# Performance work log

Hardware: AMD Instinct MI355X
Metric: run time of the kernel (lower is better)

## Reference

```python
import jax, jax.numpy as jnp
import numpy as np

TEMPERATURE = 8.0  # sqrt(d_head=64)
CLAMP = 15.0
EPS = 1e-6


def setup_inputs() -> dict:
    key = jax.random.key(0)
    kq, kk, kv, km = jax.random.split(key, 4)
    B, Lq, Lk, D = 16, 2048, 2048, 64
    q = jax.random.normal(kq, (B, Lq, D), dtype=jnp.float32)
    k = jax.random.normal(kk, (B, Lk, D), dtype=jnp.float32)
    v = jax.random.normal(kv, (B, Lk, D), dtype=jnp.float32)
    mask = jax.random.randint(km, (B, Lq, Lk), 0, 2).astype(jnp.float32)
    return {"q": q, "k": k, "v": v, "mask": mask}


def masked_softmax(x, m, axis=-1):
    # clamp -> multiply by mask -> stable exp -> multiply by mask -> normalize
    x = jnp.clip(x, -CLAMP, CLAMP)
    x = x * m
    e_x = jnp.exp(x - jnp.max(x, axis=axis, keepdims=True))
    e_x = e_x * m
    return e_x / (jnp.sum(e_x, axis=axis, keepdims=True) + EPS)


def reference(q, k, v, mask):
    # scores: [B, Lq, Lk]
    attn = jnp.einsum('bqd,bkd->bqk', q, k) / TEMPERATURE
    attn = masked_softmax(attn, mask, axis=2)
    # dropout is identity in eval mode (deterministic reference)
    output = jnp.einsum('bqk,bkd->bqd', attn, v)
    return (output, attn)
```

## Files before the change

### kernel.cpp

```cpp
#include <hip/hip_runtime.h>
#include <stdint.h>

#define NB 16
#define LQ 2048
#define LK 2048
#define DH 64
#define QT 16
#define NW 16
#define STRIP (NW * 16)
#define NIT (LK / STRIP)

typedef short bf16x8 __attribute__((ext_vector_type(8)));
typedef float f32x4 __attribute__((ext_vector_type(4)));

__device__ __forceinline__ unsigned short f2bf(float f) {
    union { float f; uint32_t u; } v; v.f = f;
    uint32_t u = v.u;
    u += 0x7FFFu + ((u >> 16) & 1u);
    return (unsigned short)(u >> 16);
}
__device__ __forceinline__ float bf2f(unsigned short h) {
    union { uint32_t u; float f; } v; v.u = ((uint32_t)h) << 16;
    return v.f;
}
__device__ __forceinline__ uint32_t pack2(float lo, float hi) {
    return (uint32_t)f2bf(lo) | ((uint32_t)f2bf(hi) << 16);
}

__global__ void convert_kernel(const float* __restrict__ q, const float* __restrict__ k,
                               const float* __restrict__ v,
                               unsigned short* __restrict__ qb,
                               unsigned short* __restrict__ kb,
                               unsigned short* __restrict__ vtb) {
    int bid = blockIdx.x;
    int tid = threadIdx.x;
    if (bid < 2048) {
        const float* src = (bid < 1024) ? q : k;
        unsigned short* dst = (bid < 1024) ? qb : kb;
        int64_t off = (int64_t)(bid & 1023) * 2048 + (int64_t)tid * 8;
        float4 a = *(const float4*)(src + off);
        float4 b4 = *(const float4*)(src + off + 4);
        uint4 o;
        o.x = pack2(a.x, a.y);
        o.y = pack2(a.z, a.w);
        o.z = pack2(b4.x, b4.y);
        o.w = pack2(b4.z, b4.w);
        *(uint4*)(dst + off) = o;
    } else {
        __shared__ unsigned short tile[64][72];
        int bid2 = bid - 2048;
        int bb = bid2 >> 5, kt = bid2 & 31;
        int k0 = kt * 64;
        int krow = tid >> 2, dc = (tid & 3) * 16;
        const float* vp = v + ((int64_t)(bb * LK) + k0 + krow) * DH + dc;
        float4 x0 = *(const float4*)(vp);
        float4 x1 = *(const float4*)(vp + 4);
        float4 x2 = *(const float4*)(vp + 8);
        float4 x3 = *(const float4*)(vp + 12);
        float vals[16] = {x0.x, x0.y, x0.z, x0.w, x1.x, x1.y, x1.z, x1.w,
                          x2.x, x2.y, x2.z, x2.w, x3.x, x3.y, x3.z, x3.w};
        #pragma unroll
        for (int i = 0; i < 16; ++i) tile[dc + i][krow] = f2bf(vals[i]);
        __syncthreads();
        int d = tid >> 2, kc = (tid & 3) * 16;
        uint4 r0 = *(const uint4*)&tile[d][kc];
        uint4 r1 = *(const uint4*)&tile[d][kc + 8];
        unsigned short* op = vtb + ((int64_t)(bb * DH) + d) * LK + k0 + kc;
        *(uint4*)op = r0;
        *(uint4*)(op + 8) = r1;
    }
}

__device__ __forceinline__ void ld_f32x4(f32x4& d, const float* p) {
    asm volatile("global_load_dwordx4 %0, %1, off" : "=v"(d) : "v"((uint64_t)p));
}
__device__ __forceinline__ void ld_bf16x8(bf16x8& d, const unsigned short* p) {
    asm volatile("global_load_dwordx4 %0, %1, off" : "=v"(d) : "v"((uint64_t)p));
}

__launch_bounds__(1024, 8)
__global__ void attn_kernel(const unsigned short* __restrict__ qb,
                            const unsigned short* __restrict__ kb,
                            const unsigned short* __restrict__ vtb,
                            const float* __restrict__ mask,
                            float* __restrict__ out, float* __restrict__ attn) {
    extern __shared__ char smem[];
    float* denom_part = (float*)(smem + QT * LK * 2);
    float* denF       = (float*)(smem + QT * LK * 2 + 1024);
    float* pp         = (float*)(smem + QT * LK * 2 + 1088);

    int bid = blockIdx.x;
    int swz = (bid & 7) * 256 + (bid >> 3);
    int b = swz >> 7;
    int q0 = (swz & 127) * QT;

    int tid = threadIdx.x;
    int lane = tid & 63;
    int wave = tid >> 6;
    int lr = lane & 15, lg = lane >> 4;

    bf16x8 qf0, qf1;
    {
        const unsigned short* qp = qb + ((int64_t)(b * LQ + q0 + lr)) * DH + 8 * lg;
        qf0 = *(const bf16x8*)qp;
        qf1 = *(const bf16x8*)(qp + 32);
    }

    float dsum = 0.f;

    {
        const unsigned short* kpw =
            kb + (int64_t)b * LK * DH + (wave * 16 + lr) * DH + 8 * lg;
        const float* mrow =
            mask + ((int64_t)(b * LQ + q0 + lr)) * LK + wave * 16 + lg * 4;

        f32x4  mk[3];
        bf16x8 ka[3], kb_[3];
        #pragma unroll
        for (int t = 0; t < 3; ++t) {
            ld_f32x4(mk[t], mrow + t * STRIP);
            ld_bf16x8(ka[t],  kpw + (int64_t)t * STRIP * DH);
            ld_bf16x8(kb_[t], kpw + (int64_t)t * STRIP * DH + 32);
        }
        #pragma unroll
        for (int kt = 0; kt < NIT; ++kt) {
            int s = kt % 3;
            if (kt < 6)
                asm volatile("s_waitcnt vmcnt(6)"
                             : "+v"(mk[s]), "+v"(ka[s]), "+v"(kb_[s]));
            else if (kt == 6)
                asm volatile("s_waitcnt vmcnt(3)"
                             : "+v"(mk[s]), "+v"(ka[s]), "+v"(kb_[s]));
            else
                asm volatile("s_waitcnt vmcnt(0)"
                             : "+v"(mk[s]), "+v"(ka[s]), "+v"(kb_[s]));
            __builtin_amdgcn_sched_barrier(0);

            f32x4 acc = {0.f, 0.f, 0.f, 0.f};
            acc = __builtin_amdgcn_mfma_f32_16x16x32_bf16(ka[s],  qf0, acc, 0, 0, 0);
            acc = __builtin_amdgcn_mfma_f32_16x16x32_bf16(kb_[s], qf1, acc, 0, 0, 0);
            unsigned short eb[4];
            #pragma unroll
            for (int j = 0; j < 4; ++j) {
                float sc = acc[j] * 0.125f;
                sc = fminf(fmaxf(sc, -15.0f), 15.0f);
                unsigned short p = f2bf(__expf(sc));
                eb[j] = (mk[s][j] != 0.f) ? p : (unsigned short)0;
                dsum += bf2f(eb[j]);
            }
            uint2 u;
            u.x = (uint32_t)eb[0] | ((uint32_t)eb[1] << 16);
            u.y = (uint32_t)eb[2] | ((uint32_t)eb[3] << 16);
            int c = kt * STRIP + wave * 16 + lg * 4;
            int byteoff = (lr * 4096 + c * 2) ^ ((lr & 7) << 4);
            *(uint2*)(smem + byteoff) = u;

            if (kt < NIT - 3) {
                ld_f32x4(mk[s], mrow + (kt + 3) * STRIP);
                ld_bf16x8(ka[s],  kpw + (int64_t)(kt + 3) * STRIP * DH);
                ld_bf16x8(kb_[s], kpw + (int64_t)(kt + 3) * STRIP * DH + 32);
            }
        }
    }

    dsum += __shfl_xor(dsum, 16);
    dsum += __shfl_xor(dsum, 32);
    if (lane < 16) denom_part[wave * 16 + lane] = dsum;
    __syncthreads();

    {
        int r = wave;
        float den = 1e-6f;
        #pragma unroll
        for (int w = 0; w < NW; ++w) den += denom_part[w * 16 + r];
        if (lane == 0) denF[r] = den;
        float inv = 1.0f / den;
        float* ap = attn + ((int64_t)(b * LQ + q0 + r)) * LK;
        int rowbase = r * 4096;
        int sw = (r & 7) << 4;
        int c0l = lane * 8;
        #pragma unroll
        for (int i = 0; i < 4; ++i) {
            int byteoff = (rowbase + (i * 512 + c0l) * 2) ^ sw;
            bf16x8 ev = *(const bf16x8*)(smem + byteoff);
            f32x4 o0, o1;
            o0[0] = bf2f((unsigned short)ev[0]) * inv;
            o0[1] = bf2f((unsigned short)ev[1]) * inv;
            o0[2] = bf2f((unsigned short)ev[2]) * inv;
            o0[3] = bf2f((unsigned short)ev[3]) * inv;
            o1[0] = bf2f((unsigned short)ev[4]) * inv;
            o1[1] = bf2f((unsigned short)ev[5]) * inv;
            o1[2] = bf2f((unsigned short)ev[6]) * inv;
            o1[3] = bf2f((unsigned short)ev[7]) * inv;
            *(f32x4*)(ap + i * 512 + c0l) = o0;
            *(f32x4*)(ap + i * 512 + c0l + 4) = o1;
        }
    }

    f32x4 pacc = {0.f, 0.f, 0.f, 0.f};
    int cw = (wave & 3) * 16, kq = wave >> 2;
    {
        const unsigned short* vp =
            vtb + ((int64_t)(b * DH + cw + lr)) * LK + kq * 512 + 8 * lg;
        int rowbase = lr * 4096;
        int sw = (lr & 7) << 4;
        int kk0 = kq * 512;
        #pragma unroll 4
        for (int kk = 0; kk < 512; kk += 32) {
            int byteoff = (rowbase + (kk0 + kk + 8 * lg) * 2) ^ sw;
            bf16x8 ef = *(const bf16x8*)(smem + byteoff);
            bf16x8 vf = *(const bf16x8*)(vp + kk);
            pacc = __builtin_amdgcn_mfma_f32_16x16x32_bf16(ef, vf, pacc, 0, 0, 0);
        }
    }
    if (kq != 0) {
        #pragma unroll
        for (int j = 0; j < 4; ++j)
            pp[((kq - 1) * 4 + (wave & 3)) * 256 + (lg * 4 + j) * 16 + lr] = pacc[j];
    }
    __syncthreads();
    if (kq == 0) {
        int c4 = wave & 3;
        #pragma unroll
        for (int j = 0; j < 4; ++j) {
            int r = lg * 4 + j;
            float den = denF[r];
            float val = pacc[j] + pp[(c4) * 256 + r * 16 + lr] +
                        pp[(4 + c4) * 256 + r * 16 + lr] +
                        pp[(8 + c4) * 256 + r * 16 + lr];
            out[((int64_t)(b * LQ + q0 + r)) * DH + cw + lr] = val / den;
        }
    }
}

extern "C" void kernel_launch(void* const* d_in, const int* in_sizes, int n_in,
                              void* d_out, int out_size, void* d_ws, size_t ws_size,
                              hipStream_t stream) {
    const float* q    = (const float*)d_in[0];
    const float* k    = (const float*)d_in[1];
    const float* v    = (const float*)d_in[2];
    const float* mask = (const float*)d_in[3];
    float* out  = (float*)d_out;
    float* attn = out + (int64_t)NB * LQ * DH;

    unsigned short* qb  = (unsigned short*)d_ws;
    unsigned short* kb  = qb + (int64_t)NB * LQ * DH;
    unsigned short* vtb = kb + (int64_t)NB * LK * DH;

    (void)hipFuncSetAttribute((const void*)attn_kernel,
                              hipFuncAttributeMaxDynamicSharedMemorySize, 78912);

    convert_kernel<<<2560, 256, 0, stream>>>(q, k, v, qb, kb, vtb);
    attn_kernel<<<2048, 1024, 78912, stream>>>(qb, kb, vtb, mask, out, attn);
}
```

Measured before the change: 215.6 us.

## Keep softmax probabilities in registers and shrink blocks to four waves

Blocks now run 4 waves instead of 16. Each wave owns a contiguous 512-key range and keeps its exponentiated scores packed in registers. The large shared-memory staging buffer is gone, and the P·V product uses 16x16x16 MFMA fed straight from the register scores, so the LDS round-trip and the extra barrier phase disappear. In exchange, register pressure rises (64 dwords of scores plus four accumulators per lane), V loads become narrower 8-byte reads, and each block has fewer waves to hide memory latency.

```diff
diff --git a/kernel.cpp b/kernel.cpp
--- a/kernel.cpp
+++ b/kernel.cpp
@@ -6,11 +6,10 @@
 #define LK 2048
 #define DH 64
 #define QT 16
-#define NW 16
-#define STRIP (NW * 16)
-#define NIT (LK / STRIP)
+#define NSTRIP 32
 
 typedef short bf16x8 __attribute__((ext_vector_type(8)));
+typedef short bf16x4 __attribute__((ext_vector_type(4)));
 typedef float f32x4 __attribute__((ext_vector_type(4)));
 
 __device__ __forceinline__ unsigned short f2bf(float f) {
@@ -78,16 +77,28 @@
     asm volatile("global_load_dwordx4 %0, %1, off" : "=v"(d) : "v"((uint64_t)p));
 }
 
-__launch_bounds__(1024, 8)
+__device__ __forceinline__ f32x4 pv_mfma(bf16x4 a, bf16x4 bfrag, f32x4 c) {
+#if defined(__has_builtin)
+#if __has_builtin(__builtin_amdgcn_mfma_f32_16x16x16bf16_1k)
+    return __builtin_amdgcn_mfma_f32_16x16x16bf16_1k(a, bfrag, c, 0, 0, 0);
+#else
+    asm("v_mfma_f32_16x16x16_bf16 %0, %1, %2, %0" : "+v"(c) : "v"(a), "v"(bfrag));
+    return c;
+#endif
+#else
+    asm("v_mfma_f32_16x16x16_bf16 %0, %1, %2, %0" : "+v"(c) : "v"(a), "v"(bfrag));
+    return c;
+#endif
+}
+
+__launch_bounds__(256, 4)
 __global__ void attn_kernel(const unsigned short* __restrict__ qb,
                             const unsigned short* __restrict__ kb,
                             const unsigned short* __restrict__ vtb,
                             const float* __restrict__ mask,
                             float* __restrict__ out, float* __restrict__ attn) {
-    extern __shared__ char smem[];
-    float* denom_part = (float*)(smem + QT * LK * 2);
-    float* denF       = (float*)(smem + QT * LK * 2 + 1024);
-    float* pp         = (float*)(smem + QT * LK * 2 + 1088);
+    __shared__ float den_part[4][16];
+    __shared__ float pp[3][4][16][16];
 
     int bid = blockIdx.x;
     int swz = (bid & 7) * 256 + (bid >> 3);
@@ -106,29 +117,30 @@
         qf1 = *(const bf16x8*)(qp + 32);
     }
 
+    const unsigned short* kpw =
+        kb + (int64_t)b * LK * DH + (wave * NSTRIP * 16 + lr) * DH + 8 * lg;
+    const float* mrow =
+        mask + ((int64_t)(b * LQ + q0 + lr)) * LK + wave * NSTRIP * 16 + lg * 4;
+
+    uint32_t es[2 * NSTRIP];
     float dsum = 0.f;
 
     {
-        const unsigned short* kpw =
-            kb + (int64_t)b * LK * DH + (wave * 16 + lr) * DH + 8 * lg;
-        const float* mrow =
-            mask + ((int64_t)(b * LQ + q0 + lr)) * LK + wave * 16 + lg * 4;
-
         f32x4  mk[3];
         bf16x8 ka[3], kb_[3];
         #pragma unroll
         for (int t = 0; t < 3; ++t) {
-            ld_f32x4(mk[t], mrow + t * STRIP);
-            ld_bf16x8(ka[t],  kpw + (int64_t)t * STRIP * DH);
-            ld_bf16x8(kb_[t], kpw + (int64_t)t * STRIP * DH + 32);
-        }
-        #pragma unroll
-        for (int kt = 0; kt < NIT; ++kt) {
+            ld_f32x4(mk[t], mrow + t * 16);
+            ld_bf16x8(ka[t],  kpw + (int64_t)t * 16 * DH);
+            ld_bf16x8(kb_[t], kpw + (int64_t)t * 16 * DH + 32);
+        }
+        #pragma unroll
+        for (int kt = 0; kt < NSTRIP; ++kt) {
             int s = kt % 3;
-            if (kt < 6)
+            if (kt < NSTRIP - 2)
                 asm volatile("s_waitcnt vmcnt(6)"
                              : "+v"(mk[s]), "+v"(ka[s]), "+v"(kb_[s]));
-            else if (kt == 6)
+            else if (kt == NSTRIP - 2)
                 asm volatile("s_waitcnt vmcnt(3)"
                              : "+v"(mk[s]), "+v"(ka[s]), "+v"(kb_[s]));
             else
@@ -148,87 +160,89 @@
                 eb[j] = (mk[s][j] != 0.f) ? p : (unsigned short)0;
                 dsum += bf2f(eb[j]);
             }
-            uint2 u;
-            u.x = (uint32_t)eb[0] | ((uint32_t)eb[1] << 16);
-            u.y = (uint32_t)eb[2] | ((uint32_t)eb[3] << 16);
-            int c = kt * STRIP + wave * 16 + lg * 4;
-            int byteoff = (lr * 4096 + c * 2) ^ ((lr & 7) << 4);
-            *(uint2*)(smem + byteoff) = u;
-
-            if (kt < NIT - 3) {
-                ld_f32x4(mk[s], mrow + (kt + 3) * STRIP);
-                ld_bf16x8(ka[s],  kpw + (int64_t)(kt + 3) * STRIP * DH);
-                ld_bf16x8(kb_[s], kpw + (int64_t)(kt + 3) * STRIP * DH + 32);
+            es[2 * kt]     = (uint32_t)eb[0] | ((uint32_t)eb[1] << 16);
+            es[2 * kt + 1] = (uint32_t)eb[2] | ((uint32_t)eb[3] << 16);
+
+            if (kt < NSTRIP - 3) {
+                ld_f32x4(mk[s], mrow + (kt + 3) * 16);
+                ld_bf16x8(ka[s],  kpw + (int64_t)(kt + 3) * 16 * DH);
+                ld_bf16x8(kb_[s], kpw + (int64_t)(kt + 3) * 16 * DH + 32);
             }
         }
     }
 
     dsum += __shfl_xor(dsum, 16);
     dsum += __shfl_xor(dsum, 32);
-    if (lane < 16) denom_part[wave * 16 + lane] = dsum;
+    if (lane < 16) den_part[wave][lane] = dsum;
     __syncthreads();
 
-    {
-        int r = wave;
-        float den = 1e-6f;
-        #pragma unroll
-        for (int w = 0; w < NW; ++w) den += denom_part[w * 16 + r];
-        if (lane == 0) denF[r] = den;
-        float inv = 1.0f / den;
-        float* ap = attn + ((int64_t)(b * LQ + q0 + r)) * LK;
-        int rowbase = r * 4096;
-        int sw = (r & 7) << 4;
-        int c0l = lane * 8;
-        #pragma unroll
-        for (int i = 0; i < 4; ++i) {
-            int byteoff = (rowbase + (i * 512 + c0l) * 2) ^ sw;
-            bf16x8 ev = *(const bf16x8*)(smem + byteoff);
-            f32x4 o0, o1;
-            o0[0] = bf2f((unsigned short)ev[0]) * inv;
-            o0[1] = bf2f((unsigned short)ev[1]) * inv;
-            o0[2] = bf2f((unsigned short)ev[2]) * inv;
-            o0[3] = bf2f((unsigned short)ev[3]) * inv;
-            o1[0] = bf2f((unsigned short)ev[4]) * inv;
-            o1[1] = bf2f((unsigned short)ev[5]) * inv;
-            o1[2] = bf2f((unsigned short)ev[6]) * inv;
-            o1[3] = bf2f((unsigned short)ev[7]) * inv;
-            *(f32x4*)(ap + i * 512 + c0l) = o0;
-            *(f32x4*)(ap + i * 512 + c0l + 4) = o1;
-        }
-    }
-
-    f32x4 pacc = {0.f, 0.f, 0.f, 0.f};
-    int cw = (wave & 3) * 16, kq = wave >> 2;
-    {
-        const unsigned short* vp =
-            vtb + ((int64_t)(b * DH + cw + lr)) * LK + kq * 512 + 8 * lg;
-        int rowbase = lr * 4096;
-        int sw = (lr & 7) << 4;
-        int kk0 = kq * 512;
-        #pragma unroll 4
-        for (int kk = 0; kk < 512; kk += 32) {
-            int byteoff = (rowbase + (kk0 + kk + 8 * lg) * 2) ^ sw;
-            bf16x8 ef = *(const bf16x8*)(smem + byteoff);
-            bf16x8 vf = *(const bf16x8*)(vp + kk);
-            pacc = __builtin_amdgcn_mfma_f32_16x16x32_bf16(ef, vf, pacc, 0, 0, 0);
-        }
-    }
-    if (kq != 0) {
-        #pragma unroll
-        for (int j = 0; j < 4; ++j)
-            pp[((kq - 1) * 4 + (wave & 3)) * 256 + (lg * 4 + j) * 16 + lr] = pacc[j];
-    }
-    __syncthreads();
-    if (kq == 0) {
-        int c4 = wave & 3;
+    float inv;
+    {
+        float den = den_part[0][lr] + den_part[1][lr] + den_part[2][lr] +
+                    den_part[3][lr] + 1e-6f;
+        inv = 1.0f / den;
+    }
+
+    f32x4 pacc0 = {0.f, 0.f, 0.f, 0.f};
+    f32x4 pacc1 = {0.f, 0.f, 0.f, 0.f};
+    f32x4 pacc2 = {0.f, 0.f, 0.f, 0.f};
+    f32x4 pacc3 = {0.f, 0.f, 0.f, 0.f};
+    {
+        float* arow = attn + ((int64_t)(b * LQ + q0 + lr)) * LK +
+                      wave * NSTRIP * 16 + lg * 4;
+        const unsigned short* vb =
+            vtb + (int64_t)b * DH * LK + lr * LK + wave * NSTRIP * 16 + lg * 4;
+        #pragma unroll
+        for (int kt = 0; kt < NSTRIP; ++kt) {
+            uint32_t w0 = es[2 * kt], w1 = es[2 * kt + 1];
+            union { uint32_t u[2]; bf16x4 v; } eu;
+            eu.u[0] = w0; eu.u[1] = w1;
+            f32x4 ao;
+            ao[0] = bf2f((unsigned short)(w0 & 0xffff)) * inv;
+            ao[1] = bf2f((unsigned short)(w0 >> 16)) * inv;
+            ao[2] = bf2f((unsigned short)(w1 & 0xffff)) * inv;
+            ao[3] = bf2f((unsigned short)(w1 >> 16)) * inv;
+            *(f32x4*)(arow + kt * 16) = ao;
+
+            const unsigned short* vk = vb + kt * 16;
+            bf16x4 vf0 = *(const bf16x4*)(vk);
+            bf16x4 vf1 = *(const bf16x4*)(vk + 16 * LK);
+            bf16x4 vf2 = *(const bf16x4*)(vk + 32 * LK);
+            bf16x4 vf3 = *(const bf16x4*)(vk + 48 * LK);
+            pacc0 = pv_mfma(eu.v, vf0, pacc0);
+            pacc1 = pv_mfma(eu.v, vf1, pacc1);
+            pacc2 = pv_mfma(eu.v, vf2, pacc2);
+            pacc3 = pv_mfma(eu.v, vf3, pacc3);
+        }
+    }
+
+    if (wave != 0) {
         #pragma unroll
         for (int j = 0; j < 4; ++j) {
             int r = lg * 4 + j;
-            float den = denF[r];
-            float val = pacc[j] + pp[(c4) * 256 + r * 16 + lr] +
-                        pp[(4 + c4) * 256 + r * 16 + lr] +
-                        pp[(8 + c4) * 256 + r * 16 + lr];
-            out[((int64_t)(b * LQ + q0 + r)) * DH + cw + lr] = val / den;
+            pp[wave - 1][0][r][lr] = pacc0[j];
+            pp[wave - 1][1][r][lr] = pacc1[j];
+            pp[wave - 1][2][r][lr] = pacc2[j];
+            pp[wave - 1][3][r][lr] = pacc3[j];
+        }
+    }
+    __syncthreads();
+    if (wave == 0) {
+        #pragma unroll
+        for (int j = 0; j < 4; ++j) {
+            int r = lg * 4 + j;
+            float den = den_part[0][r] + den_part[1][r] + den_part[2][r] +
+                        den_part[3][r] + 1e-6f;
+            float id = 1.0f / den;
+            float v0 = pacc0[j] + pp[0][0][r][lr] + pp[1][0][r][lr] + pp[2][0][r][lr];
+            float v1 = pacc1[j] + pp[0][1][r][lr] + pp[1][1][r][lr] + pp[2][1][r][lr];
+            float v2 = pacc2[j] + pp[0][2][r][lr] + pp[1][2][r][lr] + pp[2][2][r][lr];
+            float v3 = pacc3[j] + pp[0][3][r][lr] + pp[1][3][r][lr] + pp[2][3][r][lr];
+            float* op = out + ((int64_t)(b * LQ + q0 + r)) * DH + lr;
+            op[0]  = v0 * id;
+            op[16] = v1 * id;
+            op[32] = v2 * id;
+            op[48] = v3 * id;
         }
     }
 }
@@ -247,9 +261,6 @@
     unsigned short* kb  = qb + (int64_t)NB * LQ * DH;
     unsigned short* vtb = kb + (int64_t)NB * LK * DH;
 
-    (void)hipFuncSetAttribute((const void*)attn_kernel,
-                              hipFuncAttributeMaxDynamicSharedMemorySize, 78912);
-
     convert_kernel<<<2560, 256, 0, stream>>>(q, k, v, qb, kb, vtb);
-    attn_kernel<<<2048, 1024, 78912, stream>>>(qb, kb, vtb, mask, out, attn);
-}
+    attn_kernel<<<2048, 256, 0, stream>>>(qb, kb, vtb, mask, out, attn);
+}
```

Result: slower. 373.4 us (+73.2%).

## Split attention into denominator pass and fused attn/PV pass with packed mask

Applied to the files above, without the earlier changes.

The single kernel becomes two. The first computes QK scores, takes the softmax denominators, and packs the float mask into nibbles. The second recomputes the QK scores, writes normalized attention directly from registers and builds P in shared memory for the PV product. This removes the shared-memory readback and barrier before the attention write so those stores can overlap with compute. The cost is a second QK pass, an extra kernel launch and extra global traffic for the packed mask and denominators.

```diff
diff --git a/kernel.cpp b/kernel.cpp
--- a/kernel.cpp
+++ b/kernel.cpp
@@ -77,17 +77,17 @@
 __device__ __forceinline__ void ld_bf16x8(bf16x8& d, const unsigned short* p) {
     asm volatile("global_load_dwordx4 %0, %1, off" : "=v"(d) : "v"((uint64_t)p));
 }
+__device__ __forceinline__ void ld_u16(uint32_t& d, const unsigned char* p) {
+    asm volatile("global_load_ushort %0, %1, off" : "=v"(d) : "v"((uint64_t)p));
+}
 
 __launch_bounds__(1024, 8)
-__global__ void attn_kernel(const unsigned short* __restrict__ qb,
-                            const unsigned short* __restrict__ kb,
-                            const unsigned short* __restrict__ vtb,
-                            const float* __restrict__ mask,
-                            float* __restrict__ out, float* __restrict__ attn) {
-    extern __shared__ char smem[];
-    float* denom_part = (float*)(smem + QT * LK * 2);
-    float* denF       = (float*)(smem + QT * LK * 2 + 1024);
-    float* pp         = (float*)(smem + QT * LK * 2 + 1088);
+__global__ void den_kernel(const unsigned short* __restrict__ qb,
+                           const unsigned short* __restrict__ kb,
+                           const float* __restrict__ mask,
+                           unsigned char* __restrict__ maskn,
+                           float* __restrict__ den_g) {
+    __shared__ float denp[NW][16];
 
     int bid = blockIdx.x;
     int swz = (bid & 7) * 256 + (bid >> 3);
@@ -106,14 +106,15 @@
         qf1 = *(const bf16x8*)(qp + 32);
     }
 
+    const unsigned short* kpw =
+        kb + (int64_t)b * LK * DH + (wave * 16 + lr) * DH + 8 * lg;
+    const float* mrow =
+        mask + ((int64_t)(b * LQ + q0 + lr)) * LK + wave * 16 + lg * 4;
+    unsigned char* nrow =
+        maskn + ((int64_t)(b * LQ + q0 + lr)) * (LK / 2) + wave * 8 + lg * 2;
+
     float dsum = 0.f;
-
-    {
-        const unsigned short* kpw =
-            kb + (int64_t)b * LK * DH + (wave * 16 + lr) * DH + 8 * lg;
-        const float* mrow =
-            mask + ((int64_t)(b * LQ + q0 + lr)) * LK + wave * 16 + lg * 4;
-
+    {
         f32x4  mk[3];
         bf16x8 ka[3], kb_[3];
         #pragma unroll
@@ -125,10 +126,10 @@
         #pragma unroll
         for (int kt = 0; kt < NIT; ++kt) {
             int s = kt % 3;
-            if (kt < 6)
+            if (kt < NIT - 2)
                 asm volatile("s_waitcnt vmcnt(6)"
                              : "+v"(mk[s]), "+v"(ka[s]), "+v"(kb_[s]));
-            else if (kt == 6)
+            else if (kt == NIT - 2)
                 asm volatile("s_waitcnt vmcnt(3)"
                              : "+v"(mk[s]), "+v"(ka[s]), "+v"(kb_[s]));
             else
@@ -139,15 +140,109 @@
             f32x4 acc = {0.f, 0.f, 0.f, 0.f};
             acc = __builtin_amdgcn_mfma_f32_16x16x32_bf16(ka[s],  qf0, acc, 0, 0, 0);
             acc = __builtin_amdgcn_mfma_f32_16x16x32_bf16(kb_[s], qf1, acc, 0, 0, 0);
-            unsigned short eb[4];
+            uint32_t nib = 0;
             #pragma unroll
             for (int j = 0; j < 4; ++j) {
                 float sc = acc[j] * 0.125f;
                 sc = fminf(fmaxf(sc, -15.0f), 15.0f);
                 unsigned short p = f2bf(__expf(sc));
-                eb[j] = (mk[s][j] != 0.f) ? p : (unsigned short)0;
-                dsum += bf2f(eb[j]);
+                bool mz = (mk[s][j] != 0.f);
+                unsigned short eb = mz ? p : (unsigned short)0;
+                dsum += bf2f(eb);
+                nib |= (mz ? 1u : 0u) << (4 * j);
             }
+            *(unsigned short*)(nrow + kt * 128) = (unsigned short)nib;
+
+            if (kt < NIT - 3) {
+                ld_f32x4(mk[s], mrow + (kt + 3) * STRIP);
+                ld_bf16x8(ka[s],  kpw + (int64_t)(kt + 3) * STRIP * DH);
+                ld_bf16x8(kb_[s], kpw + (int64_t)(kt + 3) * STRIP * DH + 32);
+            }
+        }
+    }
+    dsum += __shfl_xor(dsum, 16);
+    dsum += __shfl_xor(dsum, 32);
+    if (lane < 16) denp[wave][lane] = dsum;
+    __syncthreads();
+    if (wave == 0 && lane < 16) {
+        float d = 1e-6f;
+        #pragma unroll
+        for (int w = 0; w < NW; ++w) d += denp[w][lane];
+        den_g[(int64_t)b * LQ + q0 + lane] = d;
+    }
+}
+
+__launch_bounds__(1024, 8)
+__global__ void attn_pv_kernel(const unsigned short* __restrict__ qb,
+                               const unsigned short* __restrict__ kb,
+                               const unsigned short* __restrict__ vtb,
+                               const unsigned char* __restrict__ maskn,
+                               const float* __restrict__ den_g,
+                               float* __restrict__ out, float* __restrict__ attn) {
+    extern __shared__ char smem[];
+    float* pp = (float*)(smem + QT * LK * 2);
+
+    int bid = blockIdx.x;
+    int swz = (bid & 7) * 256 + (bid >> 3);
+    int b = swz >> 7;
+    int q0 = (swz & 127) * QT;
+
+    int tid = threadIdx.x;
+    int lane = tid & 63;
+    int wave = tid >> 6;
+    int lr = lane & 15, lg = lane >> 4;
+
+    bf16x8 qf0, qf1;
+    {
+        const unsigned short* qp = qb + ((int64_t)(b * LQ + q0 + lr)) * DH + 8 * lg;
+        qf0 = *(const bf16x8*)qp;
+        qf1 = *(const bf16x8*)(qp + 32);
+    }
+    float inv_lr = 1.0f / den_g[(int64_t)b * LQ + q0 + lr];
+
+    const unsigned short* kpw =
+        kb + (int64_t)b * LK * DH + (wave * 16 + lr) * DH + 8 * lg;
+    const unsigned char* nrow =
+        maskn + ((int64_t)(b * LQ + q0 + lr)) * (LK / 2) + wave * 8 + lg * 2;
+    float* arow = attn + ((int64_t)(b * LQ + q0 + lr)) * LK + wave * 16 + lg * 4;
+
+    {
+        uint32_t mbk[3];
+        bf16x8 ka[3], kb_[3];
+        #pragma unroll
+        for (int t = 0; t < 3; ++t) {
+            ld_u16(mbk[t], nrow + t * 128);
+            ld_bf16x8(ka[t],  kpw + (int64_t)t * STRIP * DH);
+            ld_bf16x8(kb_[t], kpw + (int64_t)t * STRIP * DH + 32);
+        }
+        #pragma unroll
+        for (int kt = 0; kt < NIT; ++kt) {
+            int s = kt % 3;
+            if (kt < NIT - 2)
+                asm volatile("s_waitcnt vmcnt(6)"
+                             : "+v"(mbk[s]), "+v"(ka[s]), "+v"(kb_[s]));
+            else if (kt == NIT - 2)
+                asm volatile("s_waitcnt vmcnt(3)"
+                             : "+v"(mbk[s]), "+v"(ka[s]), "+v"(kb_[s]));
+            else
+                asm volatile("s_waitcnt vmcnt(0)"
+                             : "+v"(mbk[s]), "+v"(ka[s]), "+v"(kb_[s]));
+            __builtin_amdgcn_sched_barrier(0);
+
+            f32x4 acc = {0.f, 0.f, 0.f, 0.f};
+            acc = __builtin_amdgcn_mfma_f32_16x16x32_bf16(ka[s],  qf0, acc, 0, 0, 0);
+            acc = __builtin_amdgcn_mfma_f32_16x16x32_bf16(kb_[s], qf1, acc, 0, 0, 0);
+            unsigned short eb[4];
+            f32x4 ao;
+            #pragma unroll
+            for (int j = 0; j < 4; ++j) {
+                float sc = acc[j] * 0.125f;
+                sc = fminf(fmaxf(sc, -15.0f), 15.0f);
+                unsigned short p = f2bf(__expf(sc));
+                eb[j] = ((mbk[s] >> (4 * j)) & 0xFu) ? p : (unsigned short)0;
+                ao[j] = bf2f(eb[j]) * inv_lr;
+            }
+            *(f32x4*)(arow + kt * STRIP) = ao;
             uint2 u;
             u.x = (uint32_t)eb[0] | ((uint32_t)eb[1] << 16);
             u.y = (uint32_t)eb[2] | ((uint32_t)eb[3] << 16);
@@ -156,46 +251,13 @@
             *(uint2*)(smem + byteoff) = u;
 
             if (kt < NIT - 3) {
-                ld_f32x4(mk[s], mrow + (kt + 3) * STRIP);
+                ld_u16(mbk[s], nrow + (kt + 3) * 128);
                 ld_bf16x8(ka[s],  kpw + (int64_t)(kt + 3) * STRIP * DH);
                 ld_bf16x8(kb_[s], kpw + (int64_t)(kt + 3) * STRIP * DH + 32);
             }
         }
     }
-
-    dsum += __shfl_xor(dsum, 16);
-    dsum += __shfl_xor(dsum, 32);
-    if (lane < 16) denom_part[wave * 16 + lane] = dsum;
     __syncthreads();
-
-    {
-        int r = wave;
-        float den = 1e-6f;
-        #pragma unroll
-        for (int w = 0; w < NW; ++w) den += denom_part[w * 16 + r];
-        if (lane == 0) denF[r] = den;
-        float inv = 1.0f / den;
-        float* ap = attn + ((int64_t)(b * LQ + q0 + r)) * LK;
-        int rowbase = r * 4096;
-        int sw = (r & 7) << 4;
-        int c0l = lane * 8;
-        #pragma unroll
-        for (int i = 0; i < 4; ++i) {
-            int byteoff = (rowbase + (i * 512 + c0l) * 2) ^ sw;
-            bf16x8 ev = *(const bf16x8*)(smem + byteoff);
-            f32x4 o0, o1;
-            o0[0] = bf2f((unsigned short)ev[0]) * inv;
-            o0[1] = bf2f((unsigned short)ev[1]) * inv;
-            o0[2] = bf2f((unsigned short)ev[2]) * inv;
-            o0[3] = bf2f((unsigned short)ev[3]) * inv;
-            o1[0] = bf2f((unsigned short)ev[4]) * inv;
-            o1[1] = bf2f((unsigned short)ev[5]) * inv;
-            o1[2] = bf2f((unsigned short)ev[6]) * inv;
-            o1[3] = bf2f((unsigned short)ev[7]) * inv;
-            *(f32x4*)(ap + i * 512 + c0l) = o0;
-            *(f32x4*)(ap + i * 512 + c0l + 4) = o1;
-        }
-    }
 
     f32x4 pacc = {0.f, 0.f, 0.f, 0.f};
     int cw = (wave & 3) * 16, kq = wave >> 2;
@@ -224,11 +286,11 @@
         #pragma unroll
         for (int j = 0; j < 4; ++j) {
             int r = lg * 4 + j;
-            float den = denF[r];
+            float dd = den_g[(int64_t)b * LQ + q0 + r];
             float val = pacc[j] + pp[(c4) * 256 + r * 16 + lr] +
                         pp[(4 + c4) * 256 + r * 16 + lr] +
                         pp[(8 + c4) * 256 + r * 16 + lr];
-            out[((int64_t)(b * LQ + q0 + r)) * DH + cw + lr] = val / den;
+            out[((int64_t)(b * LQ + q0 + r)) * DH + cw + lr] = val / dd;
         }
     }
 }
@@ -246,10 +308,14 @@
     unsigned short* qb  = (unsigned short*)d_ws;
     unsigned short* kb  = qb + (int64_t)NB * LQ * DH;
     unsigned short* vtb = kb + (int64_t)NB * LK * DH;
-
-    (void)hipFuncSetAttribute((const void*)attn_kernel,
-                              hipFuncAttributeMaxDynamicSharedMemorySize, 78912);
+    unsigned char*  maskn = (unsigned char*)(vtb + (int64_t)NB * DH * LK);
+    float* den_g = (float*)(maskn + (int64_t)NB * LQ * (LK / 2));
+
+    (void)hipFuncSetAttribute((const void*)attn_pv_kernel,
+                              hipFuncAttributeMaxDynamicSharedMemorySize, 77824);
 
     convert_kernel<<<2560, 256, 0, stream>>>(q, k, v, qb, kb, vtb);
-    attn_kernel<<<2048, 1024, 78912, stream>>>(qb, kb, vtb, mask, out, attn);
-}
+    den_kernel<<<2048, 1024, 0, stream>>>(qb, kb, mask, maskn, den_g);
+    attn_pv_kernel<<<2048, 1024, 77824, stream>>>(qb, kb, vtb, maskn, den_g,
+                                                  out, attn);
+}
```

Result: slower. 320.3 us (+48.5%).
